# Performance work log

Hardware: AMD Instinct MI355X
Metric: run time of the kernel (lower is better)

## Reference

```python
import jax, jax.numpy as jnp
import numpy as np

EMB = 256

def setup_inputs() -> dict:
    key = jax.random.key(0)
    ks = jax.random.split(key, 7)
    c = EMB
    x = jax.random.normal(ks[0], (4, c, 64, 64), dtype=jnp.float32)
    s = 1.0 / np.sqrt(c)
    Wq = jax.random.uniform(ks[1], (c, c), jnp.float32, -s, s)
    bq = jax.random.uniform(ks[2], (c,), jnp.float32, -s, s)
    Wk = jax.random.uniform(ks[3], (c, c), jnp.float32, -s, s)
    bk = jax.random.uniform(ks[4], (c,), jnp.float32, -s, s)
    Wv = jax.random.uniform(ks[5], (c, c), jnp.float32, -s, s)
    bv = jax.random.uniform(ks[6], (c,), jnp.float32, -s, s)
    return {"x": x, "Wq": Wq, "bq": bq, "Wk": Wk, "bk": bk, "Wv": Wv, "bv": bv}

def reference(x, Wq, bq, Wk, bk, Wv, bv):
    b, c, h, w = x.shape
    scale = jnp.sqrt(jnp.float32(c))
    # [b, n, c] tokens, n = h*w
    xt = x.reshape(b, c, h * w).transpose(0, 2, 1)
    q = jnp.einsum('bnc,dc->bnd', xt, Wq) + bq
    k = jnp.einsum('bnc,dc->bnd', xt, Wk) + bk
    v = jnp.einsum('bnc,dc->bnd', xt, Wv) + bv
    dist = jnp.einsum('bnd,bmd->bnm', q, k) / scale  # [b, n, n]
    dist = jax.nn.softmax(dist, axis=-1)
    mem = jnp.einsum('bnm,bmd->bnd', dist, v)  # [b, n, c]
    # Original: permute(0,1,2) is identity, then raw view(b,c,h,w) -> reshape
    return mem.reshape(b, c, h, w)
```

## Files before the change

### kernel.cpp

```cpp
#include <hip/hip_runtime.h>

typedef __attribute__((ext_vector_type(8))) short short8;
typedef __attribute__((ext_vector_type(4))) short short4_t;
typedef __attribute__((ext_vector_type(4))) float float4_t;
typedef __attribute__((ext_vector_type(16))) float float16_t;
typedef __attribute__((ext_vector_type(2))) int int2_t;

#define NTOK 4096
#define CDIM 256
#define BPB (NTOK * CDIM)
#define C1 0.0901684400555602f

__device__ inline float bf2f(short s) {
    return __uint_as_float(((unsigned)(unsigned short)s) << 16);
}
__device__ inline short f2bf(float f) {
    unsigned u = __float_as_uint(f);
    return (short)((u + 0x7fffu + ((u >> 16) & 1u)) >> 16);
}
__device__ inline int cvtpk_bf16(float lo, float hi) {
    int d;
    asm("v_cvt_pk_bf16_f32 %0, %1, %2" : "=v"(d) : "v"(lo), "v"(hi));
    return d;
}
__device__ inline void gl_lds16(const void* g, void* l) {
    __builtin_amdgcn_global_load_lds(
        (const __attribute__((address_space(1))) unsigned int*)g,
        (__attribute__((address_space(3))) unsigned int*)l, 16, 0, 0);
}

__global__ void sniff_dtype(const unsigned* __restrict__ x, int* __restrict__ flag) {
    __shared__ int cnt;
    if (threadIdx.x == 0) cnt = 0;
    __syncthreads();
    int local = 0;
    for (int i = threadIdx.x; i < 1024; i += 256) {
        unsigned e = (x[i] >> 7) & 0xffu;
        if (e >= 100u && e <= 140u) local++;
    }
    atomicAdd(&cnt, local);
    __syncthreads();
    if (threadIdx.x == 0) flag[0] = (cnt >= 512) ? 1 : 0;
}

__global__ __launch_bounds__(256) void wprep(
    const void* __restrict__ Wq, const void* __restrict__ Wk,
    const void* __restrict__ Wv, const int* __restrict__ flag,
    short* __restrict__ Wb)
{
    const int base = (blockIdx.x * 256 + threadIdx.x) * 8;
    const int wsel = base >> 16, off = base & 65535;
    const void* W = (wsel == 0) ? Wq : (wsel == 1) ? Wk : Wv;
    short8 v;
    if (flag[0]) {
        v = *(const short8*)((const short*)W + off);
    } else {
        const float* f = (const float*)W + off;
        float4 a = *(const float4*)f;
        float4 c4 = *(const float4*)(f + 4);
        v[0]=f2bf(a.x);  v[1]=f2bf(a.y);  v[2]=f2bf(a.z);  v[3]=f2bf(a.w);
        v[4]=f2bf(c4.x); v[5]=f2bf(c4.y); v[6]=f2bf(c4.z); v[7]=f2bf(c4.w);
    }
    *(short8*)(Wb + base) = v;
}

template <bool PIN>
__global__ __launch_bounds__(256, 3) void qkv7(
    const void* __restrict__ xv, const short* __restrict__ Wb,
    const void* __restrict__ bq, const void* __restrict__ bk,
    const void* __restrict__ bv,
    const int* __restrict__ flag, int b0,
    short* __restrict__ qbase, short* __restrict__ kbase,
    short* __restrict__ vtbase)
{
    int nt, bl, wsel;
    if (PIN) {
        const int bid = blockIdx.x;
        wsel = bid >> 8;
        const int rem = bid & 255;
        bl = rem & 3; nt = rem >> 2;
    } else { nt = blockIdx.x; wsel = blockIdx.y; bl = blockIdx.z; }
    const int b = b0 + bl;
    const int n0 = nt * 64;
    const int tid = threadIdx.x;
    const int w = tid >> 6, lane = tid & 63, l15 = lane & 15, qd = lane >> 4;
    const int isbf = flag[0];

    __shared__ short obuf[64 * 264];

    short8 af[8];
    {
        const int n = n0 + 16 * w + l15;
        if (isbf) {
            const short* xs = (const short*)xv + (size_t)b * CDIM * NTOK + n;
            #pragma unroll
            for (int s = 0; s < 8; ++s) {
                short8 v;
                #pragma unroll
                for (int e = 0; e < 8; ++e)
                    v[e] = xs[(size_t)(s * 32 + qd * 8 + e) * NTOK];
                af[s] = v;
            }
        } else {
            const float* xf = (const float*)xv + (size_t)b * CDIM * NTOK + n;
            #pragma unroll
            for (int s = 0; s < 8; ++s) {
                short8 v;
                #pragma unroll
                for (int e = 0; e < 8; ++e)
                    v[e] = f2bf(xf[(size_t)(s * 32 + qd * 8 + e) * NTOK]);
                af[s] = v;
            }
        }
    }

    const short* W = Wb + wsel * 65536;
    const void* bp = (wsel == 0) ? bq : (wsel == 1) ? bk : bv;

    #pragma unroll 2
    for (int dg = 0; dg < 16; ++dg) {
        const int d = dg * 16 + l15;
        const short* wr = W + (size_t)d * 256 + qd * 8;
        short8 wv[8];
        #pragma unroll
        for (int s = 0; s < 8; ++s) wv[s] = *(const short8*)(wr + s * 32);
        float4_t acc = {0.f, 0.f, 0.f, 0.f};
        #pragma unroll
        for (int s = 0; s < 8; ++s)
            acc = __builtin_amdgcn_mfma_f32_16x16x32_bf16(af[s], wv[s], acc, 0, 0, 0);
        const float bias = isbf ? bf2f(((const short*)bp)[d])
                                : ((const float*)bp)[d];
        if (wsel < 2) {
            #pragma unroll
            for (int r = 0; r < 4; ++r)
                obuf[(16 * w + 4 * qd + r) * 264 + d] = f2bf(acc[r] + bias);
        } else {
            #pragma unroll
            for (int r = 0; r < 4; ++r)
                obuf[d * 66 + (16 * w + 4 * qd + r)] = f2bf(acc[r] + bias);
        }
    }
    __syncthreads();

    if (wsel == 0) {
        short* qdst = qbase + (size_t)bl * BPB;
        const int rl = tid >> 2;
        #pragma unroll
        for (int u = 0; u < 8; ++u) {
            const int cc = (tid & 3) + 4 * u;
            short8 vv = *(const short8*)&obuf[rl * 264 + cc * 8];
            *(short8*)(qdst + (size_t)(n0 + rl) * 256 + cc * 8) = vv;
        }
    } else if (wsel == 1) {
        short* kdst = kbase + (size_t)bl * BPB;
        const int rl = tid >> 2;
        const int tile = (n0 + rl) >> 5, rit = rl & 31;
        #pragma unroll
        for (int u = 0; u < 8; ++u) {
            const int ccp = (tid & 3) + 4 * u;
            const int cc  = ccp ^ rit;
            short8 vv = *(const short8*)&obuf[rl * 264 + cc * 8];
            *(short8*)(kdst + (size_t)tile * 8192 + rit * 256 + ccp * 8) = vv;
        }
    } else {
        short* vtdst = vtbase + (size_t)bl * BPB;
        const int d = tid;
        #pragma unroll
        for (int u = 0; u < 8; ++u) {
            short8 vv = *(const short8*)&obuf[d * 66 + u * 8];
            const int tile = (n0 >> 5) + (u >> 2), ck = u & 3;
            const int pos = ((d & 1) * 4 + ck) ^ ((d >> 1) & 7);
            *(short8*)(vtdst + (size_t)tile * 8192 + (d >> 1) * 64 + pos * 8) = vv;
        }
    }
}

__global__ __launch_bounds__(256, 2) void flash13(
    const short* __restrict__ qb, const short* __restrict__ kb,
    const short* __restrict__ vtb,
    float* __restrict__ pO, float* __restrict__ pl)
{
    const int bid = blockIdx.x;
    const int bl = bid & 3, half = (bid >> 2) & 3, qt = bid >> 4;
    const int q0 = qt * 128;
    const int tid = threadIdx.x;
    const int w = tid >> 6, lane = tid & 63, l31 = lane & 31, h = lane >> 5;

    __shared__ __align__(16) char smem[65536];
    short* kbufA = (short*)smem;
    short* vbufA = (short*)(smem + 32768);

    const short* Q  = qb  + (size_t)bl * BPB;
    const char*  Kc = (const char*)(kb  + (size_t)bl * BPB);
    const char*  Vc = (const char*)(vtb + (size_t)bl * BPB);

    short8 qf[16];
    {
        const short* qrow = Q + (size_t)(q0 + 32 * w + l31) * 256 + h * 8;
        #pragma unroll
        for (int s = 0; s < 16; ++s)
            qf[s] = *(const short8*)(qrow + s * 16);
    }

    float16_t oacc[8];
    #pragma unroll
    for (int dt = 0; dt < 8; ++dt)
        #pragma unroll
        for (int r = 0; r < 16; ++r) oacc[dt][r] = 0.f;
    float ll0 = 0.f, ll1 = 0.f, ll2 = 0.f, ll3 = 0.f;

    const int KT0 = half * 32, KT1 = KT0 + 32;

    {
        const char* ks = Kc + ((size_t)KT0 << 14);
        const char* vs = Vc + ((size_t)KT0 << 14);
        char* kd = smem + tid * 16;
        char* vd = smem + 32768 + tid * 16;
        #pragma unroll
        for (int u = 0; u < 4; ++u) {
            gl_lds16(ks + u * 4096 + tid * 16, kd + u * 4096);
            gl_lds16(vs + u * 4096 + tid * 16, vd + u * 4096);
        }
    }

    float16_t se, so;
    #pragma unroll
    for (int r = 0; r < 16; ++r) { se[r] = 0.f; so[r] = 0.f; }
    short8 pa0, pa1;

    #pragma unroll 1
    for (int kt = KT0; kt < KT1; ++kt) {
        if (kt > KT0) {
            #pragma unroll
            for (int r = 0; r < 16; ++r) se[r] = exp2f((se[r] + so[r]) * C1);
            #pragma unroll
            for (int g = 0; g < 4; ++g) {
                ll0 += se[4 * g + 0]; ll1 += se[4 * g + 1];
                ll2 += se[4 * g + 2]; ll3 += se[4 * g + 3];
            }
            {
                int x0 = cvtpk_bf16(se[0], se[1]);
                int y0 = cvtpk_bf16(se[4], se[5]);
                int z0 = cvtpk_bf16(se[2], se[3]);
                int u0 = cvtpk_bf16(se[6], se[7]);
                int2_t r1 = __builtin_amdgcn_permlane32_swap(x0, y0, false, false);
                int2_t r2 = __builtin_amdgcn_permlane32_swap(z0, u0, false, false);
                union { int i[4]; short8 s8; } uu;
                uu.i[0] = r1[0]; uu.i[1] = r2[0]; uu.i[2] = r1[1]; uu.i[3] = r2[1];
                pa0 = uu.s8;
                int x1 = cvtpk_bf16(se[8],  se[9]);
                int y1 = cvtpk_bf16(se[12], se[13]);
                int z1 = cvtpk_bf16(se[10], se[11]);
                int u1 = cvtpk_bf16(se[14], se[15]);
                int2_t r3 = __builtin_amdgcn_permlane32_swap(x1, y1, false, false);
                int2_t r4 = __builtin_amdgcn_permlane32_swap(z1, u1, false, false);
                union { int i[4]; short8 s8; } vv;
                vv.i[0] = r3[0]; vv.i[1] = r4[0]; vv.i[2] = r3[1]; vv.i[3] = r4[1];
                pa1 = vv.s8;
            }
            {
                const short* vprev = vbufA + ((kt + 1) & 1) * 8192;
                #pragma unroll
                for (int dt = 0; dt < 8; ++dt) {
                    const int d = 32 * dt + l31, d2 = d >> 1;
                    {
                        const int pos = (((d & 1) * 4 + h) ^ (d2 & 7));
                        short8 vf = *(const short8*)&vprev[d2 * 64 + pos * 8];
                        oacc[dt] = __builtin_amdgcn_mfma_f32_32x32x16_bf16(pa0, vf, oacc[dt], 0, 0, 0);
                    }
                    {
                        const int pos = (((d & 1) * 4 + 2 + h) ^ (d2 & 7));
                        short8 vf = *(const short8*)&vprev[d2 * 64 + pos * 8];
                        oacc[dt] = __builtin_amdgcn_mfma_f32_32x32x16_bf16(pa1, vf, oacc[dt], 0, 0, 0);
                    }
                }
            }
        }

        asm volatile("s_waitcnt vmcnt(0) lgkmcnt(0)" ::: "memory");
        __builtin_amdgcn_sched_barrier(0);
        __builtin_amdgcn_s_barrier();
        __builtin_amdgcn_sched_barrier(0);

        if (kt + 1 < KT1) {
            const int alt = (kt + 1) & 1;
            const char* ks = Kc + ((size_t)(kt + 1) << 14);
            const char* vs = Vc + ((size_t)(kt + 1) << 14);
            char* kd = smem + alt * 16384 + tid * 16;
            char* vd = smem + 32768 + alt * 16384 + tid * 16;
            #pragma unroll
            for (int u = 0; u < 4; ++u) {
                gl_lds16(ks + u * 4096 + tid * 16, kd + u * 4096);
                gl_lds16(vs + u * 4096 + tid * 16, vd + u * 4096);
            }
        }

        {
            const short* kcur = kbufA + (kt & 1) * 8192;
            #pragma unroll
            for (int r = 0; r < 16; ++r) { se[r] = 0.f; so[r] = 0.f; }
            #pragma unroll
            for (int j = 0; j < 8; ++j) {
                short8 ka = *(const short8*)
                    &kcur[l31 * 256 + (((4 * j + h) ^ l31) * 8)];
                se = __builtin_amdgcn_mfma_f32_32x32x16_bf16(ka, qf[2 * j], se, 0, 0, 0);
                short8 kb2 = *(const short8*)
                    &kcur[l31 * 256 + (((4 * j + 2 + h) ^ l31) * 8)];
                so = __builtin_amdgcn_mfma_f32_32x32x16_bf16(kb2, qf[2 * j + 1], so, 0, 0, 0);
            }
        }
    }

    {
        #pragma unroll
        for (int r = 0; r < 16; ++r) se[r] = exp2f((se[r] + so[r]) * C1);
        #pragma unroll
        for (int g = 0; g < 4; ++g) {
            ll0 += se[4 * g + 0]; ll1 += se[4 * g + 1];
            ll2 += se[4 * g + 2]; ll3 += se[4 * g + 3];
        }
        int x0 = cvtpk_bf16(se[0], se[1]);
        int y0 = cvtpk_bf16(se[4], se[5]);
        int z0 = cvtpk_bf16(se[2], se[3]);
        int u0 = cvtpk_bf16(se[6], se[7]);
        int2_t r1 = __builtin_amdgcn_permlane32_swap(x0, y0, false, false);
        int2_t r2 = __builtin_amdgcn_permlane32_swap(z0, u0, false, false);
        union { int i[4]; short8 s8; } uu;
        uu.i[0] = r1[0]; uu.i[1] = r2[0]; uu.i[2] = r1[1]; uu.i[3] = r2[1];
        pa0 = uu.s8;
        int x1 = cvtpk_bf16(se[8],  se[9]);
        int y1 = cvtpk_bf16(se[12], se[13]);
        int z1 = cvtpk_bf16(se[10], se[11]);
        int u1 = cvtpk_bf16(se[14], se[15]);
        int2_t r3 = __builtin_amdgcn_permlane32_swap(x1, y1, false, false);
        int2_t r4 = __builtin_amdgcn_permlane32_swap(z1, u1, false, false);
        union { int i[4]; short8 s8; } vv;
        vv.i[0] = r3[0]; vv.i[1] = r4[0]; vv.i[2] = r3[1]; vv.i[3] = r4[1];
        pa1 = vv.s8;

        const short* vlast = vbufA + ((KT1 - 1) & 1) * 8192;
        #pragma unroll
        for (int dt = 0; dt < 8; ++dt) {
            const int d = 32 * dt + l31, d2 = d >> 1;
            {
                const int pos = (((d & 1) * 4 + h) ^ (d2 & 7));
                short8 vf = *(const short8*)&vlast[d2 * 64 + pos * 8];
                oacc[dt] = __builtin_amdgcn_mfma_f32_32x32x16_bf16(pa0, vf, oacc[dt], 0, 0, 0);
            }
            {
                const int pos = (((d & 1) * 4 + 2 + h) ^ (d2 & 7));
                short8 vf = *(const short8*)&vlast[d2 * 64 + pos * 8];
                oacc[dt] = __builtin_amdgcn_mfma_f32_32x32x16_bf16(pa1, vf, oacc[dt], 0, 0, 0);
            }
        }
    }

    const size_t idx = (size_t)(bl * 32 + qt) * 4 + half;
    {
        float v2 = (ll0 + ll1) + (ll2 + ll3);
        v2 += __shfl_xor(v2, 32, 64);
        if (h == 0) pl[idx * 128 + 32 * w + l31] = v2;
    }
    float* po = pO + idx * 32768;
    #pragma unroll
    for (int dt = 0; dt < 8; ++dt) {
        #pragma unroll
        for (int r = 0; r < 16; ++r) {
            const int qrow = 32 * w + (r & 3) + 8 * (r >> 2) + 4 * h;
            po[qrow * 256 + 32 * dt + l31] = oacc[dt][r];
        }
    }
}

__global__ __launch_bounds__(256) void combine4(
    const float* __restrict__ pO, const float* __restrict__ pl,
    const int* __restrict__ flag, void* __restrict__ outv)
{
    const int tid = threadIdx.x;
    const int row = blockIdx.x * 32 + (tid >> 3);
    const int seg = (tid & 7) * 32;
    const int bl = row >> 12, n = row & 4095;
    const int qt = n >> 7, prow = n & 127;
    const size_t bidx = (size_t)(bl * 32 + qt) * 4;
    const float* P0 = pO + (bidx + 0) * 32768 + prow * 256 + seg;
    const float* P1 = P0 + 32768;
    const float* P2 = P1 + 32768;
    const float* P3 = P2 + 32768;
    const float inv = 1.0f / (pl[(bidx + 0) * 128 + prow] + pl[(bidx + 1) * 128 + prow]
                            + pl[(bidx + 2) * 128 + prow] + pl[(bidx + 3) * 128 + prow]);
    const size_t o = (size_t)row * 256 + seg;
    if (flag[0]) {
        short* op = (short*)outv;
        #pragma unroll
        for (int g = 0; g < 4; ++g) {
            float4 a  = *(const float4*)(P0 + g * 8);
            float4 a2 = *(const float4*)(P0 + g * 8 + 4);
            float4 b  = *(const float4*)(P1 + g * 8);
            float4 b2 = *(const float4*)(P1 + g * 8 + 4);
            float4 c  = *(const float4*)(P2 + g * 8);
            float4 c2 = *(const float4*)(P2 + g * 8 + 4);
            float4 d  = *(const float4*)(P3 + g * 8);
            float4 d2 = *(const float4*)(P3 + g * 8 + 4);
            short8 pk;
            pk[0]=f2bf((a.x+b.x+c.x+d.x)*inv);     pk[1]=f2bf((a.y+b.y+c.y+d.y)*inv);
            pk[2]=f2bf((a.z+b.z+c.z+d.z)*inv);     pk[3]=f2bf((a.w+b.w+c.w+d.w)*inv);
            pk[4]=f2bf((a2.x+b2.x+c2.x+d2.x)*inv); pk[5]=f2bf((a2.y+b2.y+c2.y+d2.y)*inv);
            pk[6]=f2bf((a2.z+b2.z+c2.z+d2.z)*inv); pk[7]=f2bf((a2.w+b2.w+c2.w+d2.w)*inv);
            *(short8*)(op + o + g * 8) = pk;
        }
    } else {
        float* op = (float*)outv;
        #pragma unroll
        for (int g = 0; g < 8; ++g) {
            float4 a = *(const float4*)(P0 + g * 4);
            float4 b = *(const float4*)(P1 + g * 4);
            float4 c = *(const float4*)(P2 + g * 4);
            float4 d = *(const float4*)(P3 + g * 4);
            a.x = (a.x + b.x + c.x + d.x) * inv;
            a.y = (a.y + b.y + c.y + d.y) * inv;
            a.z = (a.z + b.z + c.z + d.z) * inv;
            a.w = (a.w + b.w + c.w + d.w) * inv;
            *(float4*)(op + o + g * 4) = a;
        }
    }
}

template <bool PIN, bool SPLIT>
__global__ __launch_bounds__(256, 2) void flash12(
    int b0, const short* __restrict__ qb, const short* __restrict__ kb,
    const short* __restrict__ vtb, const int* __restrict__ flag,
    void* __restrict__ outv, float* __restrict__ pO, float* __restrict__ pl)
{
    int qt, bl, half;
    if (SPLIT) {
        const int bid = blockIdx.x;
        bl = (bid >> 1) & 3; half = bid & 1; qt = bid >> 3;
    } else if (PIN) {
        bl = blockIdx.x & 3; qt = blockIdx.x >> 2; half = 0;
    } else { qt = blockIdx.x; bl = blockIdx.z; half = 0; }

    const int b = b0 + bl;
    const int q0 = qt * 64;
    const int tid = threadIdx.x;
    const int w = tid >> 6, lane = tid & 63, l31 = lane & 31, h = lane >> 5;
    const int wi = w & 1, wh = w >> 1;

    __shared__ __align__(16) char smem[67584];
    short* kbufA = (short*)smem;
    short* vbufA = (short*)(smem + 32768);
    float* lbuf  = (float*)(smem + 66560);

    const short* Q  = qb  + (size_t)bl * BPB;
    const char*  Kc = (const char*)(kb  + (size_t)bl * BPB);
    const char*  Vc = (const char*)(vtb + (size_t)bl * BPB);

    short8 qf[16];
    {
        const short* qrow = Q + (size_t)(q0 + 32 * wh + l31) * 256 + h * 8;
        #pragma unroll
        for (int s = 0; s < 16; ++s)
            qf[s] = *(const short8*)(qrow + s * 16);
    }

    float16_t oacc[4];
    #pragma unroll
    for (int dt = 0; dt < 4; ++dt)
        #pragma unroll
        for (int r = 0; r < 16; ++r) oacc[dt][r] = 0.f;
    float ll0 = 0.f, ll1 = 0.f, ll2 = 0.f, ll3 = 0.f;

    const int KT0 = SPLIT ? half * 64 : 0;
    const int KT1 = KT0 + (SPLIT ? 64 : 128);

    {
        const char* ks = Kc + ((size_t)KT0 << 14);
        const char* vs = Vc + ((size_t)KT0 << 14);
        char* kd = smem + tid * 16;
        char* vd = smem + 32768 + tid * 16;
        #pragma unroll
        for (int u = 0; u < 4; ++u) {
            gl_lds16(ks + u * 4096 + tid * 16, kd + u * 4096);
            gl_lds16(vs + u * 4096 + tid * 16, vd + u * 4096);
        }
    }
    __syncthreads();

    short8 pa0 = {0,0,0,0,0,0,0,0}, pa1 = {0,0,0,0,0,0,0,0};

    #pragma unroll 1
    for (int kt = KT0; kt < KT1; ++kt) {
        short* kcur  = kbufA + (kt & 1) * 8192;
        short* vprev = vbufA + ((kt + 1) & 1) * 8192;

        if (kt + 1 < KT1) {
            const char* ks = Kc + ((size_t)(kt + 1) << 14);
            char* kd = smem + (((kt + 1) & 1) << 14) + tid * 16;
            #pragma unroll
            for (int u = 0; u < 4; ++u)
                gl_lds16(ks + u * 4096 + tid * 16, kd + u * 4096);
        }

        float16_t se, so;
        #pragma unroll
        for (int r = 0; r < 16; ++r) { se[r] = 0.f; so[r] = 0.f; }
        #pragma unroll
        for (int j = 0; j < 8; ++j) {
            short8 ka = *(const short8*)
                &kcur[l31 * 256 + (((4 * j + h) ^ l31) * 8)];
            se = __builtin_amdgcn_mfma_f32_32x32x16_bf16(ka, qf[2 * j], se, 0, 0, 0);
            short8 kb2 = *(const short8*)
                &kcur[l31 * 256 + (((4 * j + 2 + h) ^ l31) * 8)];
            so = __builtin_amdgcn_mfma_f32_32x32x16_bf16(kb2, qf[2 * j + 1], so, 0, 0, 0);
        }

        if (kt > KT0) {
            #pragma unroll
            for (int dt = 0; dt < 4; ++dt) {
                const int d = 128 * wi + 32 * dt + l31, d2 = d >> 1;
                {
                    const int pos = (((d & 1) * 4 + h) ^ (d2 & 7));
                    short8 vf = *(const short8*)&vprev[d2 * 64 + pos * 8];
                    oacc[dt] = __builtin_amdgcn_mfma_f32_32x32x16_bf16(pa0, vf, oacc[dt], 0, 0, 0);
                }
                {
                    const int pos = (((d & 1) * 4 + 2 + h) ^ (d2 & 7));
                    short8 vf = *(const short8*)&vprev[d2 * 64 + pos * 8];
                    oacc[dt] = __builtin_amdgcn_mfma_f32_32x32x16_bf16(pa1, vf, oacc[dt], 0, 0, 0);
                }
            }
        }

        asm volatile("s_waitcnt lgkmcnt(0)" ::: "memory");
        __builtin_amdgcn_sched_barrier(0);
        __builtin_amdgcn_s_barrier();
        __builtin_amdgcn_sched_barrier(0);

        if (kt + 1 < KT1) {
            const char* vs = Vc + ((size_t)(kt + 1) << 14);
            char* vd = smem + 32768 + (((kt + 1) & 1) << 14) + tid * 16;
            #pragma unroll
            for (int u = 0; u < 4; ++u)
                gl_lds16(vs + u * 4096 + tid * 16, vd + u * 4096);
        }

        float pf[16];
        #pragma unroll
        for (int r = 0; r < 16; ++r) pf[r] = exp2f((se[r] + so[r]) * C1);
        #pragma unroll
        for (int g = 0; g < 4; ++g) {
            ll0 += pf[4 * g + 0]; ll1 += pf[4 * g + 1];
            ll2 += pf[4 * g + 2]; ll3 += pf[4 * g + 3];
        }
        {
            int x0 = cvtpk_bf16(pf[0], pf[1]);
            int y0 = cvtpk_bf16(pf[4], pf[5]);
            int z0 = cvtpk_bf16(pf[2], pf[3]);
            int u0 = cvtpk_bf16(pf[6], pf[7]);
            int2_t r1 = __builtin_amdgcn_permlane32_swap(x0, y0, false, false);
            int2_t r2 = __builtin_amdgcn_permlane32_swap(z0, u0, false, false);
            union { int i[4]; short8 s8; } uu;
            uu.i[0] = r1[0]; uu.i[1] = r2[0]; uu.i[2] = r1[1]; uu.i[3] = r2[1];
            pa0 = uu.s8;
            int x1 = cvtpk_bf16(pf[8],  pf[9]);
            int y1 = cvtpk_bf16(pf[12], pf[13]);
            int z1 = cvtpk_bf16(pf[10], pf[11]);
            int u1 = cvtpk_bf16(pf[14], pf[15]);
            int2_t r3 = __builtin_amdgcn_permlane32_swap(x1, y1, false, false);
            int2_t r4 = __builtin_amdgcn_permlane32_swap(z1, u1, false, false);
            union { int i[4]; short8 s8; } vv;
            vv.i[0] = r3[0]; vv.i[1] = r4[0]; vv.i[2] = r3[1]; vv.i[3] = r4[1];
            pa1 = vv.s8;
        }

        __syncthreads();
    }

    {
        short* vlast = vbufA + 8192;
        #pragma unroll
        for (int dt = 0; dt < 4; ++dt) {
            const int d = 128 * wi + 32 * dt + l31, d2 = d >> 1;
            {
                const int pos = (((d & 1) * 4 + h) ^ (d2 & 7));
                short8 vf = *(const short8*)&vlast[d2 * 64 + pos * 8];
                oacc[dt] = __builtin_amdgcn_mfma_f32_32x32x16_bf16(pa0, vf, oacc[dt], 0, 0, 0);
            }
            {
                const int pos = (((d & 1) * 4 + 2 + h) ^ (d2 & 7));
                short8 vf = *(const short8*)&vlast[d2 * 64 + pos * 8];
                oacc[dt] = __builtin_amdgcn_mfma_f32_32x32x16_bf16(pa1, vf, oacc[dt], 0, 0, 0);
            }
        }
    }

    {
        float v2 = (ll0 + ll1) + (ll2 + ll3);
        v2 += __shfl_xor(v2, 32, 64);
        if (h == 0 && wi == 0) lbuf[32 * wh + l31] = v2;
    }

    if (SPLIT) {
        const size_t pidx = (size_t)(bl * 64 + qt) * 2 + half;
        float* po = pO + pidx * 16384;
        #pragma unroll
        for (int dt = 0; dt < 4; ++dt) {
            const int dim = 128 * wi + 32 * dt + l31;
            #pragma unroll
            for (int r = 0; r < 16; ++r) {
                const int qrow = 32 * wh + (r & 3) + 8 * (r >> 2) + 4 * h;
                po[qrow * 256 + dim] = oacc[dt][r];
            }
        }
        __syncthreads();
        if (tid < 64) pl[pidx * 64 + tid] = lbuf[2 * tid] * 0.f + lbuf[tid];
    } else {
        __syncthreads();
        float* obuf = (float*)smem;
        #pragma unroll
        for (int dt = 0; dt < 4; ++dt) {
            const int dim = 128 * wi + 32 * dt + l31;
            #pragma unroll
            for (int r = 0; r < 16; ++r) {
                const int qrow = 32 * wh + (r & 3) + 8 * (r >> 2) + 4 * h;
                obuf[qrow * 260 + dim] = oacc[dt][r];
            }
        }
        __syncthreads();
        {
            const int row = tid >> 2, q4 = (tid & 3) * 64;
            const float inv = 1.0f / lbuf[row];
            const float* src = obuf + row * 260 + q4;
            const size_t o = (size_t)(b * NTOK + q0 + row) * 256 + q4;
            if (flag[0]) {
                short* op = (short*)outv;
                #pragma unroll
                for (int g = 0; g < 4; ++g) {
                    float4 a  = *(const float4*)(src + g * 8);
                    float4 c4 = *(const float4*)(src + g * 8 + 4);
                    short8 pk;
                    pk[0]=f2bf(a.x*inv);  pk[1]=f2bf(a.y*inv);
                    pk[2]=f2bf(a.z*inv);  pk[3]=f2bf(a.w*inv);
                    pk[4]=f2bf(c4.x*inv); pk[5]=f2bf(c4.y*inv);
                    pk[6]=f2bf(c4.z*inv); pk[7]=f2bf(c4.w*inv);
                    *(short8*)(op + o + g * 8) = pk;
                }
            } else {
                float* op = (float*)outv;
                #pragma unroll
                for (int g = 0; g < 16; ++g) {
                    float4 a = *(const float4*)(src + g * 4);
                    a.x *= inv; a.y *= inv; a.z *= inv; a.w *= inv;
                    *(float4*)(op + o + g * 4) = a;
                }
            }
        }
    }
}

__global__ __launch_bounds__(256) void combine(
    const float* __restrict__ pO, const float* __restrict__ pl,
    const int* __restrict__ flag, void* __restrict__ outv)
{
    const int tile = blockIdx.x, tid = threadIdx.x;
    const int row = tid >> 2, seg = (tid & 3) * 64;
    const float* A = pO + (size_t)tile * 32768 + row * 256 + seg;
    const float* B = A + 16384;
    const float inv = 1.0f / (pl[tile * 128 + row] + pl[tile * 128 + 64 + row]);
    const size_t o = ((size_t)tile * 64 + row) * 256 + seg;
    if (flag[0]) {
        short* op = (short*)outv;
        #pragma unroll
        for (int g = 0; g < 8; ++g) {
            float4 a  = *(const float4*)(A + g * 8);
            float4 a2 = *(const float4*)(A + g * 8 + 4);
            float4 c  = *(const float4*)(B + g * 8);
            float4 c2 = *(const float4*)(B + g * 8 + 4);
            short8 pk;
            pk[0]=f2bf((a.x+c.x)*inv);   pk[1]=f2bf((a.y+c.y)*inv);
            pk[2]=f2bf((a.z+c.z)*inv);   pk[3]=f2bf((a.w+c.w)*inv);
            pk[4]=f2bf((a2.x+c2.x)*inv); pk[5]=f2bf((a2.y+c2.y)*inv);
            pk[6]=f2bf((a2.z+c2.z)*inv); pk[7]=f2bf((a2.w+c2.w)*inv);
            *(short8*)(op + o + g * 8) = pk;
        }
    } else {
        float* op = (float*)outv;
        #pragma unroll
        for (int g = 0; g < 16; ++g) {
            float4 a = *(const float4*)(A + g * 4);
            float4 c = *(const float4*)(B + g * 4);
            a.x = (a.x + c.x) * inv; a.y = (a.y + c.y) * inv;
            a.z = (a.z + c.z) * inv; a.w = (a.w + c.w) * inv;
            *(float4*)(op + o + g * 4) = a;
        }
    }
}

extern "C" void kernel_launch(void* const* d_in, const int* in_sizes, int n_in,
                              void* d_out, int out_size, void* d_ws, size_t ws_size,
                              hipStream_t stream)
{
    const size_t HDR = 256;
    const size_t WBB = 393216;
    const size_t TB  = (size_t)BPB * 2;
    const size_t OFF_K = HDR + WBB;
    const size_t need_prim = OFF_K + 12 * TB;
    const size_t PO2 = 33554432;
    const size_t need_s2 = need_prim + PO2 + 131072;
    const size_t PO4 = 67108864;
    const size_t need_s4 = need_prim + PO4 + 262144;

    int*   flag = (int*)d_ws;
    short* Wb   = (short*)((char*)d_ws + HDR);

    sniff_dtype<<<1, 256, 0, stream>>>((const unsigned*)d_in[0], flag);
    wprep<<<96, 256, 0, stream>>>(d_in[1], d_in[3], d_in[5], flag, Wb);

    if (ws_size >= need_prim) {
        short* kbase  = (short*)((char*)d_ws + OFF_K);
        short* vtbase = kbase  + 4 * (size_t)BPB;
        short* qbase  = vtbase + 4 * (size_t)BPB;
        qkv7<true><<<dim3(768, 1, 1), 256, 0, stream>>>(
            d_in[0], Wb, d_in[2], d_in[4], d_in[6], flag, 0,
            qbase, kbase, vtbase);
        if (ws_size >= need_s4) {
            float* pO = (float*)((char*)d_ws + need_prim);
            float* pl = (float*)((char*)d_ws + need_prim + PO4);
            flash13<<<dim3(512, 1, 1), 256, 0, stream>>>(
                qbase, kbase, vtbase, pO, pl);
            combine4<<<dim3(512, 1, 1), 256, 0, stream>>>(pO, pl, flag, d_out);
        } else if (ws_size >= need_s2) {
            float* pO = (float*)((char*)d_ws + need_prim);
            float* pl = (float*)((char*)d_ws + need_prim + PO2);
            flash12<true, true><<<dim3(512, 1, 1), 256, 0, stream>>>(
                0, qbase, kbase, vtbase, flag, d_out, pO, pl);
            combine<<<dim3(256, 1, 1), 256, 0, stream>>>(pO, pl, flag, d_out);
        } else {
            flash12<true, false><<<dim3(256, 1, 1), 256, 0, stream>>>(
                0, qbase, kbase, vtbase, flag, d_out, nullptr, nullptr);
        }
        return;
    }

    int nb = 4;
    while (nb > 1 && ws_size < OFF_K + (size_t)nb * 3 * TB) nb--;
    short* kbase  = (short*)((char*)d_ws + OFF_K);
    short* vtbase = kbase + (size_t)nb * BPB;
    short* qbase  = vtbase + (size_t)nb * BPB;

    for (int b0 = 0; b0 < 4; b0 += nb) {
        const int nbc = (4 - b0) < nb ? (4 - b0) : nb;
        qkv7<false><<<dim3(64, 3, nbc), 256, 0, stream>>>(
            d_in[0], Wb, d_in[2], d_in[4], d_in[6], flag, b0,
            qbase, kbase, vtbase);
        flash12<false, false><<<dim3(64, 1, nbc), 256, 0, stream>>>(
            b0, qbase, kbase, vtbase, flag, d_out, nullptr, nullptr);
    }
}
```

Measured before the change: 239.9 us.

## Prefetch QKV weights, raise MFMA priority, and restructure split-K combine kernel

The QKV projection kernel now software-prefetches the next 16-row weight group into registers while the current group's MFMAs run, uses 32-bit index math, and asks for 4 waves per SIMD. The flash kernel wraps its MFMA loops in s_setprio so matrix work gets issue priority. combine4 is rewritten to let each wave handle one row per step with coalesced float4 loads, looping over 16 rows with half as many blocks. A dead multiply-by-zero is dropped when the row sums are stored. Together these target load latency and memory efficiency, but they risk register pressure from the higher occupancy target and the doubled weight registers.

Result: faster. 224.7 us (-6.4%).

```diff
diff --git a/kernel.cpp b/kernel.cpp
--- a/kernel.cpp
+++ b/kernel.cpp
@@ -65,7 +65,7 @@
 }
 
 template <bool PIN>
-__global__ __launch_bounds__(256, 3) void qkv7(
+__global__ __launch_bounds__(256, 4) void qkv8(
     const void* __restrict__ xv, const short* __restrict__ Wb,
     const void* __restrict__ bq, const void* __restrict__ bk,
     const void* __restrict__ bv,
@@ -92,23 +92,23 @@
     {
         const int n = n0 + 16 * w + l15;
         if (isbf) {
-            const short* xs = (const short*)xv + (size_t)b * CDIM * NTOK + n;
+            const short* xs = (const short*)xv + (size_t)b * (CDIM * NTOK) + n;
             #pragma unroll
             for (int s = 0; s < 8; ++s) {
                 short8 v;
                 #pragma unroll
                 for (int e = 0; e < 8; ++e)
-                    v[e] = xs[(size_t)(s * 32 + qd * 8 + e) * NTOK];
+                    v[e] = xs[(s * 32 + qd * 8 + e) * NTOK];
                 af[s] = v;
             }
         } else {
-            const float* xf = (const float*)xv + (size_t)b * CDIM * NTOK + n;
+            const float* xf = (const float*)xv + (size_t)b * (CDIM * NTOK) + n;
             #pragma unroll
             for (int s = 0; s < 8; ++s) {
                 short8 v;
                 #pragma unroll
                 for (int e = 0; e < 8; ++e)
-                    v[e] = f2bf(xf[(size_t)(s * 32 + qd * 8 + e) * NTOK]);
+                    v[e] = f2bf(xf[(s * 32 + qd * 8 + e) * NTOK]);
                 af[s] = v;
             }
         }
@@ -117,13 +117,20 @@
     const short* W = Wb + wsel * 65536;
     const void* bp = (wsel == 0) ? bq : (wsel == 1) ? bk : bv;
 
-    #pragma unroll 2
+    short8 wv[8], wn[8];
+    {
+        const short* wr = W + l15 * 256 + qd * 8;
+        #pragma unroll
+        for (int s = 0; s < 8; ++s) wv[s] = *(const short8*)(wr + s * 32);
+    }
+    #pragma unroll 1
     for (int dg = 0; dg < 16; ++dg) {
         const int d = dg * 16 + l15;
-        const short* wr = W + (size_t)d * 256 + qd * 8;
-        short8 wv[8];
-        #pragma unroll
-        for (int s = 0; s < 8; ++s) wv[s] = *(const short8*)(wr + s * 32);
+        if (dg + 1 < 16) {
+            const short* wr = W + (dg * 16 + 16 + l15) * 256 + qd * 8;
+            #pragma unroll
+            for (int s = 0; s < 8; ++s) wn[s] = *(const short8*)(wr + s * 32);
+        }
         float4_t acc = {0.f, 0.f, 0.f, 0.f};
         #pragma unroll
         for (int s = 0; s < 8; ++s)
@@ -139,6 +146,8 @@
             for (int r = 0; r < 4; ++r)
                 obuf[d * 66 + (16 * w + 4 * qd + r)] = f2bf(acc[r] + bias);
         }
+        #pragma unroll
+        for (int s = 0; s < 8; ++s) wv[s] = wn[s];
     }
     __syncthreads();
 
@@ -260,6 +269,7 @@
             }
             {
                 const short* vprev = vbufA + ((kt + 1) & 1) * 8192;
+                __builtin_amdgcn_s_setprio(1);
                 #pragma unroll
                 for (int dt = 0; dt < 8; ++dt) {
                     const int d = 32 * dt + l31, d2 = d >> 1;
@@ -274,6 +284,7 @@
                         oacc[dt] = __builtin_amdgcn_mfma_f32_32x32x16_bf16(pa1, vf, oacc[dt], 0, 0, 0);
                     }
                 }
+                __builtin_amdgcn_s_setprio(0);
             }
         }
 
@@ -299,6 +310,7 @@
             const short* kcur = kbufA + (kt & 1) * 8192;
             #pragma unroll
             for (int r = 0; r < 16; ++r) { se[r] = 0.f; so[r] = 0.f; }
+            __builtin_amdgcn_s_setprio(1);
             #pragma unroll
             for (int j = 0; j < 8; ++j) {
                 short8 ka = *(const short8*)
@@ -308,6 +320,7 @@
                     &kcur[l31 * 256 + (((4 * j + 2 + h) ^ l31) * 8)];
                 so = __builtin_amdgcn_mfma_f32_32x32x16_bf16(kb2, qf[2 * j + 1], so, 0, 0, 0);
             }
+            __builtin_amdgcn_s_setprio(0);
         }
     }
 
@@ -376,51 +389,35 @@
     const float* __restrict__ pO, const float* __restrict__ pl,
     const int* __restrict__ flag, void* __restrict__ outv)
 {
-    const int tid = threadIdx.x;
-    const int row = blockIdx.x * 32 + (tid >> 3);
-    const int seg = (tid & 7) * 32;
-    const int bl = row >> 12, n = row & 4095;
-    const int qt = n >> 7, prow = n & 127;
-    const size_t bidx = (size_t)(bl * 32 + qt) * 4;
-    const float* P0 = pO + (bidx + 0) * 32768 + prow * 256 + seg;
-    const float* P1 = P0 + 32768;
-    const float* P2 = P1 + 32768;
-    const float* P3 = P2 + 32768;
-    const float inv = 1.0f / (pl[(bidx + 0) * 128 + prow] + pl[(bidx + 1) * 128 + prow]
-                            + pl[(bidx + 2) * 128 + prow] + pl[(bidx + 3) * 128 + prow]);
-    const size_t o = (size_t)row * 256 + seg;
-    if (flag[0]) {
-        short* op = (short*)outv;
-        #pragma unroll
-        for (int g = 0; g < 4; ++g) {
-            float4 a  = *(const float4*)(P0 + g * 8);
-            float4 a2 = *(const float4*)(P0 + g * 8 + 4);
-            float4 b  = *(const float4*)(P1 + g * 8);
-            float4 b2 = *(const float4*)(P1 + g * 8 + 4);
-            float4 c  = *(const float4*)(P2 + g * 8);
-            float4 c2 = *(const float4*)(P2 + g * 8 + 4);
-            float4 d  = *(const float4*)(P3 + g * 8);
-            float4 d2 = *(const float4*)(P3 + g * 8 + 4);
-            short8 pk;
-            pk[0]=f2bf((a.x+b.x+c.x+d.x)*inv);     pk[1]=f2bf((a.y+b.y+c.y+d.y)*inv);
-            pk[2]=f2bf((a.z+b.z+c.z+d.z)*inv);     pk[3]=f2bf((a.w+b.w+c.w+d.w)*inv);
-            pk[4]=f2bf((a2.x+b2.x+c2.x+d2.x)*inv); pk[5]=f2bf((a2.y+b2.y+c2.y+d2.y)*inv);
-            pk[6]=f2bf((a2.z+b2.z+c2.z+d2.z)*inv); pk[7]=f2bf((a2.w+b2.w+c2.w+d2.w)*inv);
-            *(short8*)(op + o + g * 8) = pk;
-        }
-    } else {
-        float* op = (float*)outv;
-        #pragma unroll
-        for (int g = 0; g < 8; ++g) {
-            float4 a = *(const float4*)(P0 + g * 4);
-            float4 b = *(const float4*)(P1 + g * 4);
-            float4 c = *(const float4*)(P2 + g * 4);
-            float4 d = *(const float4*)(P3 + g * 4);
-            a.x = (a.x + b.x + c.x + d.x) * inv;
-            a.y = (a.y + b.y + c.y + d.y) * inv;
-            a.z = (a.z + b.z + c.z + d.z) * inv;
-            a.w = (a.w + b.w + c.w + d.w) * inv;
-            *(float4*)(op + o + g * 4) = a;
+    const int tid = threadIdx.x, w = tid >> 6, lane = tid & 63;
+    const int isbf = flag[0];
+    #pragma unroll 1
+    for (int st = 0; st < 16; ++st) {
+        const int row = blockIdx.x * 64 + st * 4 + w;
+        const int bl = row >> 12, n = row & 4095;
+        const int qt = n >> 7, prow = n & 127;
+        const size_t bidx = (size_t)(bl * 32 + qt) * 4;
+        const float* P0 = pO + bidx * 32768 + prow * 256 + lane * 4;
+        float4 a = *(const float4*)P0;
+        float4 b = *(const float4*)(P0 + 32768);
+        float4 c = *(const float4*)(P0 + 65536);
+        float4 d = *(const float4*)(P0 + 98304);
+        const float inv = 1.0f /
+            (pl[(bidx + 0) * 128 + prow] + pl[(bidx + 1) * 128 + prow] +
+             pl[(bidx + 2) * 128 + prow] + pl[(bidx + 3) * 128 + prow]);
+        float4 r;
+        r.x = (a.x + b.x + c.x + d.x) * inv;
+        r.y = (a.y + b.y + c.y + d.y) * inv;
+        r.z = (a.z + b.z + c.z + d.z) * inv;
+        r.w = (a.w + b.w + c.w + d.w) * inv;
+        const size_t o = (size_t)row * 256 + lane * 4;
+        if (isbf) {
+            short4_t pk;
+            pk[0] = f2bf(r.x); pk[1] = f2bf(r.y);
+            pk[2] = f2bf(r.z); pk[3] = f2bf(r.w);
+            *(short4_t*)((short*)outv + o) = pk;
+        } else {
+            *(float4*)((float*)outv + o) = r;
         }
     }
 }
@@ -612,7 +609,7 @@
             }
         }
         __syncthreads();
-        if (tid < 64) pl[pidx * 64 + tid] = lbuf[2 * tid] * 0.f + lbuf[tid];
+        if (tid < 64) pl[pidx * 64 + tid] = lbuf[tid];
     } else {
         __syncthreads();
         float* obuf = (float*)smem;
@@ -657,7 +654,7 @@
     }
 }
 
-__global__ __launch_bounds__(256) void combine(
+__global__ __launch_bounds__(256) void combine2(
     const float* __restrict__ pO, const float* __restrict__ pl,
     const int* __restrict__ flag, void* __restrict__ outv)
 {
@@ -719,7 +716,7 @@
         short* kbase  = (short*)((char*)d_ws + OFF_K);
         short* vtbase = kbase  + 4 * (size_t)BPB;
         short* qbase  = vtbase + 4 * (size_t)BPB;
-        qkv7<true><<<dim3(768, 1, 1), 256, 0, stream>>>(
+        qkv8<true><<<dim3(768, 1, 1), 256, 0, stream>>>(
             d_in[0], Wb, d_in[2], d_in[4], d_in[6], flag, 0,
             qbase, kbase, vtbase);
         if (ws_size >= need_s4) {
@@ -727,13 +724,13 @@
             float* pl = (float*)((char*)d_ws + need_prim + PO4);
             flash13<<<dim3(512, 1, 1), 256, 0, stream>>>(
                 qbase, kbase, vtbase, pO, pl);
-            combine4<<<dim3(512, 1, 1), 256, 0, stream>>>(pO, pl, flag, d_out);
+            combine4<<<dim3(256, 1, 1), 256, 0, stream>>>(pO, pl, flag, d_out);
         } else if (ws_size >= need_s2) {
             float* pO = (float*)((char*)d_ws + need_prim);
             float* pl = (float*)((char*)d_ws + need_prim + PO2);
             flash12<true, true><<<dim3(512, 1, 1), 256, 0, stream>>>(
                 0, qbase, kbase, vtbase, flag, d_out, pO, pl);
-            combine<<<dim3(256, 1, 1), 256, 0, stream>>>(pO, pl, flag, d_out);
+            combine2<<<dim3(256, 1, 1), 256, 0, stream>>>(pO, pl, flag, d_out);
         } else {
             flash12<true, false><<<dim3(256, 1, 1), 256, 0, stream>>>(
                 0, qbase, kbase, vtbase, flag, d_out, nullptr, nullptr);
@@ -749,7 +746,7 @@
 
     for (int b0 = 0; b0 < 4; b0 += nb) {
         const int nbc = (4 - b0) < nb ? (4 - b0) : nb;
-        qkv7<false><<<dim3(64, 3, nbc), 256, 0, stream>>>(
+        qkv8<false><<<dim3(64, 3, nbc), 256, 0, stream>>>(
             d_in[0], Wb, d_in[2], d_in[4], d_in[6], flag, b0,
             qbase, kbase, vtbase);
         flash12<false, false><<<dim3(64, 1, nbc), 256, 0, stream>>>(
```
